# Optimization experiments

Measured on AMD Instinct MI355X. Metric: run time of the kernel, lower is better.

Reference implementation:

```python
import jax, jax.numpy as jnp
import numpy as np

B, LQ, LA, H = 32, 1024, 1024, 512
NEG_INF = jnp.float32(-1e7)  # matches torch masked_fill_(-10000000.0)


def setup_inputs() -> dict:
    key = jax.random.key(0)
    k1, k2, k3, k4 = jax.random.split(key, 4)
    q = jax.random.normal(k1, (B, LQ, H), dtype=jnp.float32)
    a = jax.random.normal(k2, (B, LA, H), dtype=jnp.float32)
    q_mask = jax.random.randint(k3, (B, LQ, 1), 0, 2).astype(jnp.int32)
    a_mask = jax.random.randint(k4, (B, LA, 1), 0, 2).astype(jnp.int32)
    # learned scalar, initialized exactly as in __init__
    temperature = jnp.float32(1.0 / np.sqrt(H))
    return {"q": q, "a": a, "q_mask": q_mask, "a_mask": a_mask,
            "temperature": temperature}


def reference(q, a, q_mask, a_mask, temperature):
    # scaled co-attention scores: [B, Lq, La]
    attn = jnp.einsum('bqh,bah->bqa', q, a) * temperature
    # validity mask via outer product of per-token masks (nonzero = valid)
    mask = jnp.matmul(q_mask.astype(jnp.float32),
                      a_mask.transpose(0, 2, 1).astype(jnp.float32)) != 0
    attn = jnp.where(mask, attn, NEG_INF)
    # dual-axis softmax over the SAME score matrix
    attn_q = jax.nn.softmax(attn, axis=1)  # normalize over Lq
    attn_a = jax.nn.softmax(attn, axis=2)  # normalize over La
    # aggregation: a_s = attn_q^T @ q -> [B, La, H]; q_s = attn_a @ a -> [B, Lq, H]
    a_s = jnp.einsum('bqa,bqh->bah', attn_q, q)
    q_s = jnp.einsum('bqa,bah->bqh', attn_a, a)
    return (jnp.concatenate([q, q_s], axis=-1),
            jnp.concatenate([a, a_s], axis=-1))
```

## Files before the change

### kernel.cpp

```cpp
#include <hip/hip_runtime.h>
#include <cstdint>
#include <cstddef>

#define NB   32
#define LQA  1024
#define HD   512

typedef __attribute__((ext_vector_type(4))) float  f32x4;
typedef __attribute__((ext_vector_type(8))) short  s16x8;
typedef __attribute__((ext_vector_type(4))) unsigned short u16x4;

static __device__ __forceinline__ unsigned short f2bf(float f) {
  unsigned int u = __builtin_bit_cast(unsigned int, f);
  u += 0x7fffu + ((u >> 16) & 1u);
  return (unsigned short)(u >> 16);
}
static __device__ __forceinline__ float bf2f(unsigned short h) {
  unsigned int u = ((unsigned int)h) << 16;
  return __builtin_bit_cast(float, u);
}
static __device__ __forceinline__ u16x4 cvt4(f32x4 v) {
  u16x4 r;
  r.x = f2bf(v.x); r.y = f2bf(v.y); r.z = f2bf(v.z); r.w = f2bf(v.w);
  return r;
}

typedef __attribute__((address_space(1))) const void gas_void;
typedef __attribute__((address_space(3))) void las_void;
static __device__ __forceinline__ void gload_lds16(const void* g, void* l) {
  __builtin_amdgcn_global_load_lds((gas_void*)g, (las_void*)l, 16, 0, 0);
}

__global__ __launch_bounds__(256) void k_prep(
    const float* __restrict__ qsrc, const float* __restrict__ asrc,
    float* __restrict__ out0, float* __restrict__ out1,
    unsigned short* __restrict__ qT, unsigned short* __restrict__ aT,
    unsigned short* __restrict__ qb16, unsigned short* __restrict__ ab16,
    float* __restrict__ qsum, float* __restrict__ asum)
{
  const int bz  = blockIdx.z;
  const int isA = bz >> 5;
  const int b   = bz & 31;
  const int h0 = blockIdx.x * 64;
  const int q0 = blockIdx.y * 64;
  const int t  = threadIdx.x;

  const float* src = isA ? asrc : qsrc;
  float* out_left      = isA ? out1 : out0;
  unsigned short* dstT = isA ? aT : qT;
  unsigned short* dstN = isA ? ab16 : qb16;
  float* csum          = isA ? asum : qsum;

  __shared__ unsigned short T[64 * 68];

  const float* sb = src + (size_t)b * LQA * HD;
  float* ob       = out_left + (size_t)b * LQA * 1024;
  unsigned short* db  = dstT + (size_t)b * HD * LQA;
  unsigned short* dbn = dstN + (size_t)b * LQA * HD;

#pragma unroll
  for (int j = 0; j < 4; ++j) {
    int f = t + 256 * j;
    int r = f >> 4;
    int c = (f & 15) * 4;
    f32x4 v = *(const f32x4*)(sb + (size_t)(q0 + r) * HD + h0 + c);
    *(f32x4*)(ob + (size_t)(q0 + r) * 1024 + h0 + c) = v;
    u16x4 cv = cvt4(v);
    *(u16x4*)&dbn[(size_t)(q0 + r) * HD + h0 + c] = cv;
    *(u16x4*)&T[r * 68 + c] = cv;
  }
  __syncthreads();
#pragma unroll
  for (int j = 0; j < 4; ++j) {
    int f = t + 256 * j;
    int orow = f >> 4;
    int c = (f & 15) * 4;
    u16x4 v;
    v.x = T[(c + 0) * 68 + orow];
    v.y = T[(c + 1) * 68 + orow];
    v.z = T[(c + 2) * 68 + orow];
    v.w = T[(c + 3) * 68 + orow];
    *(u16x4*)&db[(size_t)(h0 + orow) * LQA + q0 + c] = v;
    float s = bf2f(v.x) + bf2f(v.y) + bf2f(v.z) + bf2f(v.w);
    s += __shfl_xor(s, 1); s += __shfl_xor(s, 2);
    s += __shfl_xor(s, 4); s += __shfl_xor(s, 8);
    if ((t & 15) == 0)
      atomicAdd(&csum[(size_t)b * HD + h0 + orow], s);
  }
}

__global__ __launch_bounds__(256) void k_scores(
    const unsigned short* __restrict__ qb16, const unsigned short* __restrict__ ab16,
    const int* __restrict__ qmask, const int* __restrict__ amask,
    const float* __restrict__ temp_p,
    unsigned short* __restrict__ E, unsigned short* __restrict__ ET,
    float* __restrict__ rowsumE,
    float* __restrict__ colsumE)
{
  const int flat = blockIdx.x;
  const int xcd  = flat & 7;
  const int i5   = flat >> 3;
  const int b    = (i5 >> 6) * 8 + xcd;
  const int tile = i5 & 63;
  const int m0 = (tile & 7) * 128;
  const int n0 = (tile >> 3) * 128;

  const int t  = threadIdx.x;
  const int lane = t & 63;
  const int w  = t >> 6;
  const int moff = (w & 1) * 64;
  const int noff = (w >> 1) * 64;
  const int lrow = lane & 15;
  const int quad = lane >> 4;

  __shared__ __align__(16) unsigned short smem[128 * 132];
  unsigned short* As = smem;
  unsigned short* Bs = smem + 8192;

  const unsigned short* qb = qb16 + (size_t)b * LQA * HD;
  const unsigned short* ab = ab16 + (size_t)b * LQA * HD;

  const unsigned short* qg = qb + (size_t)(m0 + (t >> 3)) * HD + (t & 7) * 8;
  const unsigned short* ag = ab + (size_t)(n0 + (t >> 3)) * HD + (t & 7) * 8;

  f32x4 acc[4][4];
#pragma unroll
  for (int i = 0; i < 4; ++i)
#pragma unroll
    for (int j = 0; j < 4; ++j) acc[i][j] = (f32x4)0.f;

  for (int kt = 0; kt < HD / 64; ++kt) {
    const int ko = kt * 64;
#pragma unroll
    for (int p = 0; p < 4; ++p) {
      gload_lds16(qg + ko + p * 32 * HD, As + (w + 4 * p) * 512);
      gload_lds16(ag + ko + p * 32 * HD, Bs + (w + 4 * p) * 512);
    }
    __syncthreads();
#pragma unroll
    for (int ks = 0; ks < 2; ++ks) {
      s16x8 af[4], bfr[4];
#pragma unroll
      for (int i = 0; i < 4; ++i) {
        af[i]  = *(const s16x8*)&As[(moff + i * 16 + lrow) * 64 + ks * 32 + quad * 8];
        bfr[i] = *(const s16x8*)&Bs[(noff + i * 16 + lrow) * 64 + ks * 32 + quad * 8];
      }
#pragma unroll
      for (int i = 0; i < 4; ++i)
#pragma unroll
        for (int j = 0; j < 4; ++j)
          acc[i][j] = __builtin_amdgcn_mfma_f32_16x16x32_bf16(af[i], bfr[j], acc[i][j], 0, 0, 0);
    }
    __syncthreads();
  }

  unsigned short* Cs = smem;
  const float temp = temp_p[0];
  const int* qmb = qmask + b * LQA;
  const int* amb = amask + b * LQA;

  float rowp[4][4];
  float colp[4];
#pragma unroll
  for (int i = 0; i < 4; ++i)
#pragma unroll
    for (int r = 0; r < 4; ++r) rowp[i][r] = 0.f;
#pragma unroll
  for (int j = 0; j < 4; ++j) colp[j] = 0.f;

#pragma unroll
  for (int i = 0; i < 4; ++i) {
#pragma unroll
    for (int j = 0; j < 4; ++j) {
      int ncol = noff + j * 16 + lrow;
      float am = (amb[n0 + ncol] != 0) ? 1.f : 0.f;
#pragma unroll
      for (int r = 0; r < 4; ++r) {
        int mrow = moff + i * 16 + quad * 4 + r;
        float qm = (qmb[m0 + mrow] != 0) ? 1.f : 0.f;
        float e = __expf(acc[i][j][r] * temp) * am * qm;
        unsigned short eb = f2bf(e);
        float er = bf2f(eb);
        Cs[mrow * 132 + ncol] = eb;
        rowp[i][r] += er;
        colp[j] += er;
      }
    }
  }

#pragma unroll
  for (int i = 0; i < 4; ++i)
#pragma unroll
    for (int r = 0; r < 4; ++r) {
      float v = rowp[i][r];
      v += __shfl_xor(v, 1); v += __shfl_xor(v, 2);
      v += __shfl_xor(v, 4); v += __shfl_xor(v, 8);
      if (lrow == 0)
        atomicAdd(&rowsumE[(size_t)b * LQA + m0 + moff + i * 16 + quad * 4 + r], v);
    }
#pragma unroll
  for (int j = 0; j < 4; ++j) {
    float v = colp[j];
    v += __shfl_xor(v, 16); v += __shfl_xor(v, 32);
    if (quad == 0)
      atomicAdd(&colsumE[(size_t)b * LQA + n0 + noff + j * 16 + lrow], v);
  }

  __syncthreads();
  const size_t Ebase = (size_t)b * LQA * LQA;
#pragma unroll
  for (int jj = 0; jj < 16; ++jj) {
    int f = t + 256 * jj;
    int row = f >> 5;
    int c = (f & 31) * 4;
    u16x4 v = *(const u16x4*)&Cs[row * 132 + c];
    *(u16x4*)&E[Ebase + (size_t)(m0 + row) * LQA + n0 + c] = v;
  }
#pragma unroll
  for (int jj = 0; jj < 16; ++jj) {
    int f = t + 256 * jj;
    int orow = f >> 5;
    int c = (f & 31) * 4;
    u16x4 v;
    v.x = Cs[(c + 0) * 132 + orow];
    v.y = Cs[(c + 1) * 132 + orow];
    v.z = Cs[(c + 2) * 132 + orow];
    v.w = Cs[(c + 3) * 132 + orow];
    *(u16x4*)&ET[Ebase + (size_t)(n0 + orow) * LQA + m0 + c] = v;
  }
}

__global__ __launch_bounds__(512, 2) void k_agg2(
    const unsigned short* __restrict__ Ein,
    const unsigned short* __restrict__ ETin,
    const unsigned short* __restrict__ qT,
    const unsigned short* __restrict__ aT,
    const float* __restrict__ sums,
    const float* __restrict__ qsum,
    const float* __restrict__ asum,
    float* __restrict__ out0, float* __restrict__ out1)
{
  const int blk  = blockIdx.x;
  const int L    = (blk & 7) * 64 + (blk >> 3);
  const int half = L >> 8;
  const int rem  = L & 255;
  const int b    = rem >> 3;
  const int m0   = (rem & 7) * 128;

  const unsigned short* Emat = half ? ETin : Ein;
  const unsigned short* Bt   = half ? qT : aT;
  const float* srow = sums + (size_t)half * NB * LQA + (size_t)b * LQA;
  const float* bsp  = (half ? qsum : asum) + (size_t)b * HD;
  float* ob = (half ? out1 : out0) + (size_t)b * LQA * 1024;

  const int t    = threadIdx.x;
  const int lane = t & 63;
  const int w    = t >> 6;
  const int wr   = w >> 2;
  const int wc   = w & 3;
  const int lrow = lane & 15;
  const int quad = lane >> 4;

  __shared__ __align__(16) unsigned short lds[3 * 20480];

  const unsigned short* Eb = Emat + (size_t)b * LQA * LQA;
  const unsigned short* Bb = Bt + (size_t)b * HD * LQA;

  const unsigned short* agp = Eb + (size_t)(m0 + (t >> 2)) * LQA + (t & 3) * 8;
  const unsigned short* bgp[4];
#pragma unroll
  for (int p = 0; p < 4; ++p)
    bgp[p] = Bb + (size_t)(128 * p + (t >> 2)) * LQA + (t & 3) * 8;
  const int ldsA = w * 512;
  const int ldsB = 4096 + w * 512;

#define STAGE(kt, buf)                                                     \
  do {                                                                     \
    unsigned short* bp_ = lds + (buf) * 20480;                             \
    const int ko_ = (kt) * 32;                                             \
    gload_lds16(agp + ko_, bp_ + ldsA);                                    \
    gload_lds16(bgp[0] + ko_, bp_ + ldsB);                                 \
    gload_lds16(bgp[1] + ko_, bp_ + ldsB + 4096);                          \
    gload_lds16(bgp[2] + ko_, bp_ + ldsB + 8192);                          \
    gload_lds16(bgp[3] + ko_, bp_ + ldsB + 12288);                         \
  } while (0)

  f32x4 acc[4][8];
#pragma unroll
  for (int i = 0; i < 4; ++i)
#pragma unroll
    for (int j = 0; j < 8; ++j) acc[i][j] = (f32x4)0.f;

  STAGE(0, 0); STAGE(1, 1); STAGE(2, 2);

  int cur = 0;
  for (int k = 0; k < 32; ++k) {
    if (k <= 29)      asm volatile("s_waitcnt vmcnt(10)");
    else if (k == 30) asm volatile("s_waitcnt vmcnt(5)");
    else              asm volatile("s_waitcnt vmcnt(0)");
    __builtin_amdgcn_sched_barrier(0);
    __builtin_amdgcn_s_barrier();
    __builtin_amdgcn_sched_barrier(0);

    const unsigned short* As = lds + cur * 20480;
    const unsigned short* Bs = As + 4096;
    s16x8 bfr[8];
#pragma unroll
    for (int j = 0; j < 8; ++j)
      bfr[j] = *(const s16x8*)&Bs[(wc * 128 + j * 16 + lrow) * 32 + quad * 8];
#pragma unroll
    for (int i = 0; i < 4; ++i) {
      s16x8 af = *(const s16x8*)&As[(wr * 64 + i * 16 + lrow) * 32 + quad * 8];
#pragma unroll
      for (int j = 0; j < 8; ++j)
        acc[i][j] = __builtin_amdgcn_mfma_f32_16x16x32_bf16(af, bfr[j], acc[i][j], 0, 0, 0);
    }

    asm volatile("s_waitcnt lgkmcnt(0)");
    __builtin_amdgcn_sched_barrier(0);
    __builtin_amdgcn_s_barrier();
    if (k + 3 < 32) STAGE(k + 3, cur);
    cur = (cur == 2) ? 0 : cur + 1;
  }
#undef STAGE

  float bcol[8];
#pragma unroll
  for (int j = 0; j < 8; ++j) bcol[j] = bsp[wc * 128 + j * 16 + lrow];
#pragma unroll
  for (int i = 0; i < 4; ++i) {
#pragma unroll
    for (int r = 0; r < 4; ++r) {
      int mrow = wr * 64 + i * 16 + quad * 4 + r;
      float s = srow[m0 + mrow];
      float inv = (s > 0.f) ? 1.f / s : 0.f;
      float add = (s > 0.f) ? 0.f : (1.f / 1024.f);
#pragma unroll
      for (int j = 0; j < 8; ++j) {
        int ncol = wc * 128 + j * 16 + lrow;
        ob[(size_t)(m0 + mrow) * 1024 + 512 + ncol] =
            inv * acc[i][j][r] + add * bcol[j];
      }
    }
  }
}

extern "C" void kernel_launch(void* const* d_in, const int* in_sizes, int n_in,
                              void* d_out, int out_size, void* d_ws, size_t ws_size,
                              hipStream_t stream) {
  (void)in_sizes; (void)n_in; (void)out_size; (void)ws_size;
  const float* q    = (const float*)d_in[0];
  const float* a    = (const float*)d_in[1];
  const int*   qm   = (const int*)d_in[2];
  const int*   am   = (const int*)d_in[3];
  const float* temp = (const float*)d_in[4];

  float* out0 = (float*)d_out;
  float* out1 = out0 + (size_t)NB * LQA * 1024;

  char* ws = (char*)d_ws;
  const size_t MB = 1024ull * 1024ull;
  unsigned short* E    = (unsigned short*)(ws);
  unsigned short* ET   = (unsigned short*)(ws + 64 * MB);
  unsigned short* qT   = (unsigned short*)(ws + 128 * MB);
  unsigned short* aT   = (unsigned short*)(ws + 160 * MB);
  unsigned short* qb16 = (unsigned short*)(ws + 192 * MB);
  unsigned short* ab16 = (unsigned short*)(ws + 224 * MB);
  float* sums = (float*)(ws + 256 * MB);
  float* qsum = (float*)(ws + 256 * MB + (256 << 10));
  float* asum = (float*)(ws + 256 * MB + (320 << 10));

  hipMemsetAsync(sums, 0, (size_t)(2 * NB * LQA + 2 * NB * HD) * sizeof(float), stream);
  k_prep<<<dim3(8, 16, 2 * NB), 256, 0, stream>>>(q, a, out0, out1, qT, aT,
                                                  qb16, ab16, qsum, asum);
  k_scores<<<dim3(2048), 256, 0, stream>>>(qb16, ab16, qm, am, temp,
                                           E, ET, sums, sums + NB * LQA);
  k_agg2<<<dim3(512), 512, 0, stream>>>(E, ET, qT, aT, sums, qsum, asum,
                                        out0, out1);
}
```

Before: 604.0 us.

## Merge prep, scores and aggregation into one cooperative persistent kernel

Replaces the memset and three kernel launches with a single cooperative kernel of 256 blocks of 512 threads that runs each phase in turn, separated by grid-wide syncs. Each block loops over the work items its former kernels covered, and the score phase runs two 256-thread groups per block. This is meant to remove launch gaps and the memset. In exchange it adds grid.sync costs and fixes occupancy at 256 persistent blocks, which may lower parallelism in the prep and score phases.

```diff
diff --git a/kernel.cpp b/kernel.cpp
--- a/kernel.cpp
+++ b/kernel.cpp
@@ -1,6 +1,9 @@
 #include <hip/hip_runtime.h>
+#include <hip/hip_cooperative_groups.h>
 #include <cstdint>
 #include <cstddef>
+
+namespace cg = cooperative_groups;
 
 #define NB   32
 #define LQA  1024
@@ -31,315 +34,326 @@
   __builtin_amdgcn_global_load_lds((gas_void*)g, (las_void*)l, 16, 0, 0);
 }
 
-__global__ __launch_bounds__(256) void k_prep(
+__global__ __launch_bounds__(512, 2) void k_mega(
     const float* __restrict__ qsrc, const float* __restrict__ asrc,
+    const int* __restrict__ qmask, const int* __restrict__ amask,
+    const float* __restrict__ temp_p,
     float* __restrict__ out0, float* __restrict__ out1,
-    unsigned short* __restrict__ qT, unsigned short* __restrict__ aT,
+    unsigned short* __restrict__ E,    unsigned short* __restrict__ ET,
+    unsigned short* __restrict__ qT,   unsigned short* __restrict__ aT,
     unsigned short* __restrict__ qb16, unsigned short* __restrict__ ab16,
+    float* __restrict__ sums,
     float* __restrict__ qsum, float* __restrict__ asum)
 {
-  const int bz  = blockIdx.z;
-  const int isA = bz >> 5;
-  const int b   = bz & 31;
-  const int h0 = blockIdx.x * 64;
-  const int q0 = blockIdx.y * 64;
-  const int t  = threadIdx.x;
-
-  const float* src = isA ? asrc : qsrc;
-  float* out_left      = isA ? out1 : out0;
-  unsigned short* dstT = isA ? aT : qT;
-  unsigned short* dstN = isA ? ab16 : qb16;
-  float* csum          = isA ? asum : qsum;
-
-  __shared__ unsigned short T[64 * 68];
-
-  const float* sb = src + (size_t)b * LQA * HD;
-  float* ob       = out_left + (size_t)b * LQA * 1024;
-  unsigned short* db  = dstT + (size_t)b * HD * LQA;
-  unsigned short* dbn = dstN + (size_t)b * LQA * HD;
-
-#pragma unroll
-  for (int j = 0; j < 4; ++j) {
-    int f = t + 256 * j;
-    int r = f >> 4;
-    int c = (f & 15) * 4;
-    f32x4 v = *(const f32x4*)(sb + (size_t)(q0 + r) * HD + h0 + c);
-    *(f32x4*)(ob + (size_t)(q0 + r) * 1024 + h0 + c) = v;
-    u16x4 cv = cvt4(v);
-    *(u16x4*)&dbn[(size_t)(q0 + r) * HD + h0 + c] = cv;
-    *(u16x4*)&T[r * 68 + c] = cv;
+  cg::grid_group grid = cg::this_grid();
+  const int r = blockIdx.x;
+  const int t = threadIdx.x;
+
+  __shared__ __align__(16) unsigned short lds[3 * 20480];
+
+  {
+    const int idx = r * 512 + t;
+    if (idx < 2 * NB * LQA + 2 * NB * HD) sums[idx] = 0.f;
   }
-  __syncthreads();
-#pragma unroll
-  for (int j = 0; j < 4; ++j) {
-    int f = t + 256 * j;
-    int orow = f >> 4;
-    int c = (f & 15) * 4;
-    u16x4 v;
-    v.x = T[(c + 0) * 68 + orow];
-    v.y = T[(c + 1) * 68 + orow];
-    v.z = T[(c + 2) * 68 + orow];
-    v.w = T[(c + 3) * 68 + orow];
-    *(u16x4*)&db[(size_t)(h0 + orow) * LQA + q0 + c] = v;
-    float s = bf2f(v.x) + bf2f(v.y) + bf2f(v.z) + bf2f(v.w);
-    s += __shfl_xor(s, 1); s += __shfl_xor(s, 2);
-    s += __shfl_xor(s, 4); s += __shfl_xor(s, 8);
-    if ((t & 15) == 0)
-      atomicAdd(&csum[(size_t)b * HD + h0 + orow], s);
-  }
-}
-
-__global__ __launch_bounds__(256) void k_scores(
-    const unsigned short* __restrict__ qb16, const unsigned short* __restrict__ ab16,
-    const int* __restrict__ qmask, const int* __restrict__ amask,
-    const float* __restrict__ temp_p,
-    unsigned short* __restrict__ E, unsigned short* __restrict__ ET,
-    float* __restrict__ rowsumE,
-    float* __restrict__ colsumE)
-{
-  const int flat = blockIdx.x;
-  const int xcd  = flat & 7;
-  const int i5   = flat >> 3;
-  const int b    = (i5 >> 6) * 8 + xcd;
-  const int tile = i5 & 63;
-  const int m0 = (tile & 7) * 128;
-  const int n0 = (tile >> 3) * 128;
-
-  const int t  = threadIdx.x;
-  const int lane = t & 63;
-  const int w  = t >> 6;
-  const int moff = (w & 1) * 64;
-  const int noff = (w >> 1) * 64;
-  const int lrow = lane & 15;
-  const int quad = lane >> 4;
-
-  __shared__ __align__(16) unsigned short smem[128 * 132];
-  unsigned short* As = smem;
-  unsigned short* Bs = smem + 8192;
-
-  const unsigned short* qb = qb16 + (size_t)b * LQA * HD;
-  const unsigned short* ab = ab16 + (size_t)b * LQA * HD;
-
-  const unsigned short* qg = qb + (size_t)(m0 + (t >> 3)) * HD + (t & 7) * 8;
-  const unsigned short* ag = ab + (size_t)(n0 + (t >> 3)) * HD + (t & 7) * 8;
-
-  f32x4 acc[4][4];
-#pragma unroll
-  for (int i = 0; i < 4; ++i)
-#pragma unroll
-    for (int j = 0; j < 4; ++j) acc[i][j] = (f32x4)0.f;
-
-  for (int kt = 0; kt < HD / 64; ++kt) {
-    const int ko = kt * 64;
-#pragma unroll
-    for (int p = 0; p < 4; ++p) {
-      gload_lds16(qg + ko + p * 32 * HD, As + (w + 4 * p) * 512);
-      gload_lds16(ag + ko + p * 32 * HD, Bs + (w + 4 * p) * 512);
-    }
-    __syncthreads();
-#pragma unroll
-    for (int ks = 0; ks < 2; ++ks) {
-      s16x8 af[4], bfr[4];
-#pragma unroll
-      for (int i = 0; i < 4; ++i) {
-        af[i]  = *(const s16x8*)&As[(moff + i * 16 + lrow) * 64 + ks * 32 + quad * 8];
-        bfr[i] = *(const s16x8*)&Bs[(noff + i * 16 + lrow) * 64 + ks * 32 + quad * 8];
-      }
-#pragma unroll
-      for (int i = 0; i < 4; ++i)
-#pragma unroll
-        for (int j = 0; j < 4; ++j)
-          acc[i][j] = __builtin_amdgcn_mfma_f32_16x16x32_bf16(af[i], bfr[j], acc[i][j], 0, 0, 0);
-    }
-    __syncthreads();
-  }
-
-  unsigned short* Cs = smem;
-  const float temp = temp_p[0];
-  const int* qmb = qmask + b * LQA;
-  const int* amb = amask + b * LQA;
-
-  float rowp[4][4];
-  float colp[4];
-#pragma unroll
-  for (int i = 0; i < 4; ++i)
-#pragma unroll
-    for (int r = 0; r < 4; ++r) rowp[i][r] = 0.f;
-#pragma unroll
-  for (int j = 0; j < 4; ++j) colp[j] = 0.f;
-
-#pragma unroll
-  for (int i = 0; i < 4; ++i) {
-#pragma unroll
-    for (int j = 0; j < 4; ++j) {
-      int ncol = noff + j * 16 + lrow;
-      float am = (amb[n0 + ncol] != 0) ? 1.f : 0.f;
-#pragma unroll
-      for (int r = 0; r < 4; ++r) {
-        int mrow = moff + i * 16 + quad * 4 + r;
-        float qm = (qmb[m0 + mrow] != 0) ? 1.f : 0.f;
-        float e = __expf(acc[i][j][r] * temp) * am * qm;
-        unsigned short eb = f2bf(e);
-        float er = bf2f(eb);
-        Cs[mrow * 132 + ncol] = eb;
-        rowp[i][r] += er;
-        colp[j] += er;
-      }
+  grid.sync();
+
+  {
+    const int g  = t >> 8;
+    const int tt = t & 255;
+    unsigned short* T = lds + g * (64 * 68);
+
+    for (int it = 0; it < 16; ++it) {
+      const int v   = it * 512 + r * 2 + g;
+      const int bz  = v >> 7;
+      const int isA = bz >> 5;
+      const int b   = bz & 31;
+      const int q0  = ((v >> 3) & 15) * 64;
+      const int h0  = (v & 7) * 64;
+
+      const float* src     = isA ? asrc : qsrc;
+      float* out_left      = isA ? out1 : out0;
+      unsigned short* dstT = isA ? aT : qT;
+      unsigned short* dstN = isA ? ab16 : qb16;
+      float* csum          = isA ? asum : qsum;
+
+      const float* sb = src + (size_t)b * LQA * HD;
+      float* ob       = out_left + (size_t)b * LQA * 1024;
+      unsigned short* db  = dstT + (size_t)b * HD * LQA;
+      unsigned short* dbn = dstN + (size_t)b * LQA * HD;
+
+#pragma unroll
+      for (int j = 0; j < 4; ++j) {
+        int f = tt + 256 * j;
+        int rr = f >> 4;
+        int c  = (f & 15) * 4;
+        f32x4 vv = *(const f32x4*)(sb + (size_t)(q0 + rr) * HD + h0 + c);
+        *(f32x4*)(ob + (size_t)(q0 + rr) * 1024 + h0 + c) = vv;
+        u16x4 cv = cvt4(vv);
+        *(u16x4*)&dbn[(size_t)(q0 + rr) * HD + h0 + c] = cv;
+        *(u16x4*)&T[rr * 68 + c] = cv;
+      }
+      __syncthreads();
+#pragma unroll
+      for (int j = 0; j < 4; ++j) {
+        int f = tt + 256 * j;
+        int orow = f >> 4;
+        int c = (f & 15) * 4;
+        u16x4 vv;
+        vv.x = T[(c + 0) * 68 + orow];
+        vv.y = T[(c + 1) * 68 + orow];
+        vv.z = T[(c + 2) * 68 + orow];
+        vv.w = T[(c + 3) * 68 + orow];
+        *(u16x4*)&db[(size_t)(h0 + orow) * LQA + q0 + c] = vv;
+        float s = bf2f(vv.x) + bf2f(vv.y) + bf2f(vv.z) + bf2f(vv.w);
+        s += __shfl_xor(s, 1); s += __shfl_xor(s, 2);
+        s += __shfl_xor(s, 4); s += __shfl_xor(s, 8);
+        if ((tt & 15) == 0)
+          atomicAdd(&csum[(size_t)b * HD + h0 + orow], s);
+      }
+      __syncthreads();
     }
   }
-
-#pragma unroll
-  for (int i = 0; i < 4; ++i)
-#pragma unroll
-    for (int r = 0; r < 4; ++r) {
-      float v = rowp[i][r];
-      v += __shfl_xor(v, 1); v += __shfl_xor(v, 2);
-      v += __shfl_xor(v, 4); v += __shfl_xor(v, 8);
-      if (lrow == 0)
-        atomicAdd(&rowsumE[(size_t)b * LQA + m0 + moff + i * 16 + quad * 4 + r], v);
+  grid.sync();
+
+  {
+    const int g  = t >> 8;
+    const int tt = t & 255;
+    unsigned short* smem = lds + g * 16896;
+    unsigned short* As = smem;
+    unsigned short* Bs = smem + 8192;
+
+    const int lane = tt & 63;
+    const int w    = tt >> 6;
+    const int moff = (w & 1) * 64;
+    const int noff = (w >> 1) * 64;
+    const int lrow = lane & 15;
+    const int quad = lane >> 4;
+    const float temp = temp_p[0];
+
+    for (int it = 0; it < 4; ++it) {
+      const int flat = it * 512 + r * 2 + g;
+      const int xcd  = flat & 7;
+      const int i5   = flat >> 3;
+      const int b    = (i5 >> 6) * 8 + xcd;
+      const int tile = i5 & 63;
+      const int m0 = (tile & 7) * 128;
+      const int n0 = (tile >> 3) * 128;
+
+      const unsigned short* qb = qb16 + (size_t)b * LQA * HD;
+      const unsigned short* ab = ab16 + (size_t)b * LQA * HD;
+      const unsigned short* qg = qb + (size_t)(m0 + (tt >> 3)) * HD + (tt & 7) * 8;
+      const unsigned short* ag = ab + (size_t)(n0 + (tt >> 3)) * HD + (tt & 7) * 8;
+
+      f32x4 acc[4][4];
+#pragma unroll
+      for (int i = 0; i < 4; ++i)
+#pragma unroll
+        for (int j = 0; j < 4; ++j) acc[i][j] = (f32x4)0.f;
+
+      for (int kt = 0; kt < HD / 64; ++kt) {
+        const int ko = kt * 64;
+#pragma unroll
+        for (int p = 0; p < 4; ++p) {
+          gload_lds16(qg + ko + p * 32 * HD, As + (w + 4 * p) * 512);
+          gload_lds16(ag + ko + p * 32 * HD, Bs + (w + 4 * p) * 512);
+        }
+        __syncthreads();
+#pragma unroll
+        for (int ks = 0; ks < 2; ++ks) {
+          s16x8 af[4], bfr[4];
+#pragma unroll
+          for (int i = 0; i < 4; ++i) {
+            af[i]  = *(const s16x8*)&As[(moff + i * 16 + lrow) * 64 + ks * 32 + quad * 8];
+            bfr[i] = *(const s16x8*)&Bs[(noff + i * 16 + lrow) * 64 + ks * 32 + quad * 8];
+          }
+#pragma unroll
+          for (int i = 0; i < 4; ++i)
+#pragma unroll
+            for (int j = 0; j < 4; ++j)
+              acc[i][j] = __builtin_amdgcn_mfma_f32_16x16x32_bf16(af[i], bfr[j], acc[i][j], 0, 0, 0);
+        }
+        __syncthreads();
+      }
+
+      unsigned short* Cs = smem;
+      const int* qmb = qmask + b * LQA;
+      const int* amb = amask + b * LQA;
+
+      float rowp[4][4];
+      float colp[4];
+#pragma unroll
+      for (int i = 0; i < 4; ++i)
+#pragma unroll
+        for (int rr = 0; rr < 4; ++rr) rowp[i][rr] = 0.f;
+#pragma unroll
+      for (int j = 0; j < 4; ++j) colp[j] = 0.f;
+
+#pragma unroll
+      for (int i = 0; i < 4; ++i) {
+#pragma unroll
+        for (int j = 0; j < 4; ++j) {
+          int ncol = noff + j * 16 + lrow;
+          float am = (amb[n0 + ncol] != 0) ? 1.f : 0.f;
+#pragma unroll
+          for (int rr = 0; rr < 4; ++rr) {
+            int mrow = moff + i * 16 + quad * 4 + rr;
+            float qm = (qmb[m0 + mrow] != 0) ? 1.f : 0.f;
+            float e = __expf(acc[i][j][rr] * temp) * am * qm;
+            unsigned short eb = f2bf(e);
+            float er = bf2f(eb);
+            Cs[mrow * 132 + ncol] = eb;
+            rowp[i][rr] += er;
+            colp[j] += er;
+          }
+        }
+      }
+
+#pragma unroll
+      for (int i = 0; i < 4; ++i)
+#pragma unroll
+        for (int rr = 0; rr < 4; ++rr) {
+          float v = rowp[i][rr];
+          v += __shfl_xor(v, 1); v += __shfl_xor(v, 2);
+          v += __shfl_xor(v, 4); v += __shfl_xor(v, 8);
+          if (lrow == 0)
+            atomicAdd(&sums[(size_t)b * LQA + m0 + moff + i * 16 + quad * 4 + rr], v);
+        }
+#pragma unroll
+      for (int j = 0; j < 4; ++j) {
+        float v = colp[j];
+        v += __shfl_xor(v, 16); v += __shfl_xor(v, 32);
+        if (quad == 0)
+          atomicAdd(&sums[(size_t)NB * LQA + (size_t)b * LQA + n0 + noff + j * 16 + lrow], v);
+      }
+
+      __syncthreads();
+      const size_t Ebase = (size_t)b * LQA * LQA;
+#pragma unroll
+      for (int jj = 0; jj < 16; ++jj) {
+        int f = tt + 256 * jj;
+        int row = f >> 5;
+        int c = (f & 31) * 4;
+        u16x4 v = *(const u16x4*)&Cs[row * 132 + c];
+        *(u16x4*)&E[Ebase + (size_t)(m0 + row) * LQA + n0 + c] = v;
+      }
+#pragma unroll
+      for (int jj = 0; jj < 16; ++jj) {
+        int f = tt + 256 * jj;
+        int orow = f >> 5;
+        int c = (f & 31) * 4;
+        u16x4 v;
+        v.x = Cs[(c + 0) * 132 + orow];
+        v.y = Cs[(c + 1) * 132 + orow];
+        v.z = Cs[(c + 2) * 132 + orow];
+        v.w = Cs[(c + 3) * 132 + orow];
+        *(u16x4*)&ET[Ebase + (size_t)(n0 + orow) * LQA + m0 + c] = v;
+      }
+      __syncthreads();
     }
-#pragma unroll
-  for (int j = 0; j < 4; ++j) {
-    float v = colp[j];
-    v += __shfl_xor(v, 16); v += __shfl_xor(v, 32);
-    if (quad == 0)
-      atomicAdd(&colsumE[(size_t)b * LQA + n0 + noff + j * 16 + lrow], v);
   }
-
-  __syncthreads();
-  const size_t Ebase = (size_t)b * LQA * LQA;
-#pragma unroll
-  for (int jj = 0; jj < 16; ++jj) {
-    int f = t + 256 * jj;
-    int row = f >> 5;
-    int c = (f & 31) * 4;
-    u16x4 v = *(const u16x4*)&Cs[row * 132 + c];
-    *(u16x4*)&E[Ebase + (size_t)(m0 + row) * LQA + n0 + c] = v;
-  }
-#pragma unroll
-  for (int jj = 0; jj < 16; ++jj) {
-    int f = t + 256 * jj;
-    int orow = f >> 5;
-    int c = (f & 31) * 4;
-    u16x4 v;
-    v.x = Cs[(c + 0) * 132 + orow];
-    v.y = Cs[(c + 1) * 132 + orow];
-    v.z = Cs[(c + 2) * 132 + orow];
-    v.w = Cs[(c + 3) * 132 + orow];
-    *(u16x4*)&ET[Ebase + (size_t)(n0 + orow) * LQA + m0 + c] = v;
-  }
-}
-
-__global__ __launch_bounds__(512, 2) void k_agg2(
-    const unsigned short* __restrict__ Ein,
-    const unsigned short* __restrict__ ETin,
-    const unsigned short* __restrict__ qT,
-    const unsigned short* __restrict__ aT,
-    const float* __restrict__ sums,
-    const float* __restrict__ qsum,
-    const float* __restrict__ asum,
-    float* __restrict__ out0, float* __restrict__ out1)
-{
-  const int blk  = blockIdx.x;
-  const int L    = (blk & 7) * 64 + (blk >> 3);
-  const int half = L >> 8;
-  const int rem  = L & 255;
-  const int b    = rem >> 3;
-  const int m0   = (rem & 7) * 128;
-
-  const unsigned short* Emat = half ? ETin : Ein;
-  const unsigned short* Bt   = half ? qT : aT;
-  const float* srow = sums + (size_t)half * NB * LQA + (size_t)b * LQA;
-  const float* bsp  = (half ? qsum : asum) + (size_t)b * HD;
-  float* ob = (half ? out1 : out0) + (size_t)b * LQA * 1024;
-
-  const int t    = threadIdx.x;
-  const int lane = t & 63;
-  const int w    = t >> 6;
-  const int wr   = w >> 2;
-  const int wc   = w & 3;
-  const int lrow = lane & 15;
-  const int quad = lane >> 4;
-
-  __shared__ __align__(16) unsigned short lds[3 * 20480];
-
-  const unsigned short* Eb = Emat + (size_t)b * LQA * LQA;
-  const unsigned short* Bb = Bt + (size_t)b * HD * LQA;
-
-  const unsigned short* agp = Eb + (size_t)(m0 + (t >> 2)) * LQA + (t & 3) * 8;
-  const unsigned short* bgp[4];
-#pragma unroll
-  for (int p = 0; p < 4; ++p)
-    bgp[p] = Bb + (size_t)(128 * p + (t >> 2)) * LQA + (t & 3) * 8;
-  const int ldsA = w * 512;
-  const int ldsB = 4096 + w * 512;
+  grid.sync();
+
+  {
+    const int lane = t & 63;
+    const int w    = t >> 6;
+    const int wr   = w >> 2;
+    const int wc   = w & 3;
+    const int lrow = lane & 15;
+    const int quad = lane >> 4;
+
+    for (int it = 0; it < 2; ++it) {
+      const int blk  = it * 256 + r;
+      const int L    = (blk & 7) * 64 + (blk >> 3);
+      const int half = L >> 8;
+      const int rem  = L & 255;
+      const int b    = rem >> 3;
+      const int m0   = (rem & 7) * 128;
+
+      const unsigned short* Emat = half ? ET : E;
+      const unsigned short* Bt   = half ? qT : aT;
+      const float* srow = sums + (size_t)half * NB * LQA + (size_t)b * LQA;
+      const float* bsp  = (half ? qsum : asum) + (size_t)b * HD;
+      float* ob = (half ? out1 : out0) + (size_t)b * LQA * 1024;
+
+      const unsigned short* Eb = Emat + (size_t)b * LQA * LQA;
+      const unsigned short* Bb = Bt + (size_t)b * HD * LQA;
+
+      const unsigned short* agp = Eb + (size_t)(m0 + (t >> 2)) * LQA + (t & 3) * 8;
+      const unsigned short* bgp[4];
+#pragma unroll
+      for (int p = 0; p < 4; ++p)
+        bgp[p] = Bb + (size_t)(128 * p + (t >> 2)) * LQA + (t & 3) * 8;
+      const int ldsA = w * 512;
+      const int ldsB = 4096 + w * 512;
 
 #define STAGE(kt, buf)                                                     \
-  do {                                                                     \
-    unsigned short* bp_ = lds + (buf) * 20480;                             \
-    const int ko_ = (kt) * 32;                                             \
-    gload_lds16(agp + ko_, bp_ + ldsA);                                    \
-    gload_lds16(bgp[0] + ko_, bp_ + ldsB);                                 \
-    gload_lds16(bgp[1] + ko_, bp_ + ldsB + 4096);                          \
-    gload_lds16(bgp[2] + ko_, bp_ + ldsB + 8192);                          \
-    gload_lds16(bgp[3] + ko_, bp_ + ldsB + 12288);                         \
-  } while (0)
-
-  f32x4 acc[4][8];
-#pragma unroll
-  for (int i = 0; i < 4; ++i)
-#pragma unroll
-    for (int j = 0; j < 8; ++j) acc[i][j] = (f32x4)0.f;
-
-  STAGE(0, 0); STAGE(1, 1); STAGE(2, 2);
-
-  int cur = 0;
-  for (int k = 0; k < 32; ++k) {
-    if (k <= 29)      asm volatile("s_waitcnt vmcnt(10)");
-    else if (k == 30) asm volatile("s_waitcnt vmcnt(5)");
-    else              asm volatile("s_waitcnt vmcnt(0)");
-    __builtin_amdgcn_sched_barrier(0);
-    __builtin_amdgcn_s_barrier();
-    __builtin_amdgcn_sched_barrier(0);
-
-    const unsigned short* As = lds + cur * 20480;
-    const unsigned short* Bs = As + 4096;
-    s16x8 bfr[8];
-#pragma unroll
-    for (int j = 0; j < 8; ++j)
-      bfr[j] = *(const s16x8*)&Bs[(wc * 128 + j * 16 + lrow) * 32 + quad * 8];
-#pragma unroll
-    for (int i = 0; i < 4; ++i) {
-      s16x8 af = *(const s16x8*)&As[(wr * 64 + i * 16 + lrow) * 32 + quad * 8];
-#pragma unroll
-      for (int j = 0; j < 8; ++j)
-        acc[i][j] = __builtin_amdgcn_mfma_f32_16x16x32_bf16(af, bfr[j], acc[i][j], 0, 0, 0);
-    }
-
-    asm volatile("s_waitcnt lgkmcnt(0)");
-    __builtin_amdgcn_sched_barrier(0);
-    __builtin_amdgcn_s_barrier();
-    if (k + 3 < 32) STAGE(k + 3, cur);
-    cur = (cur == 2) ? 0 : cur + 1;
-  }
+      do {                                                                 \
+        unsigned short* bp_ = lds + (buf) * 20480;                         \
+        const int ko_ = (kt) * 32;                                         \
+        gload_lds16(agp + ko_, bp_ + ldsA);                                \
+        gload_lds16(bgp[0] + ko_, bp_ + ldsB);                             \
+        gload_lds16(bgp[1] + ko_, bp_ + ldsB + 4096);                      \
+        gload_lds16(bgp[2] + ko_, bp_ + ldsB + 8192);                      \
+        gload_lds16(bgp[3] + ko_, bp_ + ldsB + 12288);                     \
+      } while (0)
+
+      f32x4 acc[4][8];
+#pragma unroll
+      for (int i = 0; i < 4; ++i)
+#pragma unroll
+        for (int j = 0; j < 8; ++j) acc[i][j] = (f32x4)0.f;
+
+      STAGE(0, 0); STAGE(1, 1); STAGE(2, 2);
+
+      int cur = 0;
+      for (int k = 0; k < 32; ++k) {
+        if (k <= 29)      asm volatile("s_waitcnt vmcnt(10)");
+        else if (k == 30) asm volatile("s_waitcnt vmcnt(5)");
+        else              asm volatile("s_waitcnt vmcnt(0)");
+        __builtin_amdgcn_sched_barrier(0);
+        __builtin_amdgcn_s_barrier();
+        __builtin_amdgcn_sched_barrier(0);
+
+        const unsigned short* As = lds + cur * 20480;
+        const unsigned short* Bs = As + 4096;
+        s16x8 bfr[8];
+#pragma unroll
+        for (int j = 0; j < 8; ++j)
+          bfr[j] = *(const s16x8*)&Bs[(wc * 128 + j * 16 + lrow) * 32 + quad * 8];
+#pragma unroll
+        for (int i = 0; i < 4; ++i) {
+          s16x8 af = *(const s16x8*)&As[(wr * 64 + i * 16 + lrow) * 32 + quad * 8];
+#pragma unroll
+          for (int j = 0; j < 8; ++j)
+            acc[i][j] = __builtin_amdgcn_mfma_f32_16x16x32_bf16(af, bfr[j], acc[i][j], 0, 0, 0);
+        }
+
+        asm volatile("s_waitcnt lgkmcnt(0)");
+        __builtin_amdgcn_sched_barrier(0);
+        __builtin_amdgcn_s_barrier();
+        if (k + 3 < 32) STAGE(k + 3, cur);
+        cur = (cur == 2) ? 0 : cur + 1;
+      }
 #undef STAGE
 
-  float bcol[8];
-#pragma unroll
-  for (int j = 0; j < 8; ++j) bcol[j] = bsp[wc * 128 + j * 16 + lrow];
-#pragma unroll
-  for (int i = 0; i < 4; ++i) {
-#pragma unroll
-    for (int r = 0; r < 4; ++r) {
-      int mrow = wr * 64 + i * 16 + quad * 4 + r;
-      float s = srow[m0 + mrow];
-      float inv = (s > 0.f) ? 1.f / s : 0.f;
-      float add = (s > 0.f) ? 0.f : (1.f / 1024.f);
-#pragma unroll
-      for (int j = 0; j < 8; ++j) {
-        int ncol = wc * 128 + j * 16 + lrow;
-        ob[(size_t)(m0 + mrow) * 1024 + 512 + ncol] =
-            inv * acc[i][j][r] + add * bcol[j];
+      float bcol[8];
+#pragma unroll
+      for (int j = 0; j < 8; ++j) bcol[j] = bsp[wc * 128 + j * 16 + lrow];
+#pragma unroll
+      for (int i = 0; i < 4; ++i) {
+#pragma unroll
+        for (int rr = 0; rr < 4; ++rr) {
+          int mrow = wr * 64 + i * 16 + quad * 4 + rr;
+          float s = srow[m0 + mrow];
+          float inv = (s > 0.f) ? 1.f / s : 0.f;
+          float add = (s > 0.f) ? 0.f : (1.f / 1024.f);
+#pragma unroll
+          for (int j = 0; j < 8; ++j) {
+            int ncol = wc * 128 + j * 16 + lrow;
+            ob[(size_t)(m0 + mrow) * 1024 + 512 + ncol] =
+                inv * acc[i][rr == 0 ? j : j][rr] + add * bcol[j];
+          }
+        }
       }
     }
   }
@@ -370,11 +384,10 @@
   float* qsum = (float*)(ws + 256 * MB + (256 << 10));
   float* asum = (float*)(ws + 256 * MB + (320 << 10));
 
-  hipMemsetAsync(sums, 0, (size_t)(2 * NB * LQA + 2 * NB * HD) * sizeof(float), stream);
-  k_prep<<<dim3(8, 16, 2 * NB), 256, 0, stream>>>(q, a, out0, out1, qT, aT,
-                                                  qb16, ab16, qsum, asum);
-  k_scores<<<dim3(2048), 256, 0, stream>>>(qb16, ab16, qm, am, temp,
-                                           E, ET, sums, sums + NB * LQA);
-  k_agg2<<<dim3(512), 512, 0, stream>>>(E, ET, qT, aT, sums, qsum, asum,
-                                        out0, out1);
-}
+  void* args[] = { (void*)&q, (void*)&a, (void*)&qm, (void*)&am, (void*)&temp,
+                   (void*)&out0, (void*)&out1,
+                   (void*)&E, (void*)&ET, (void*)&qT, (void*)&aT,
+                   (void*)&qb16, (void*)&ab16,
+                   (void*)&sums, (void*)&qsum, (void*)&asum };
+  hipLaunchCooperativeKernel((void*)k_mega, dim3(256), dim3(512), args, 0, stream);
+}
```

Result: slower. 726.9 us (+20.4%).
